# Performance work log

Measured on AMD Instinct MI355X. Metric: run time of the kernel, lower is better.

The kernel has to match this reference:

```python
import jax, jax.numpy as jnp
import numpy as np
import math

HEADS = 12
D_MODEL = 768
D_K = D_MODEL // HEADS


def setup_inputs() -> dict:
    key = jax.random.key(0)
    ks = jax.random.split(key, 11)
    B, S, D = 2, 2048, D_MODEL
    p = 0.02
    return {
        "query": jax.random.normal(ks[0], (B, S, D), jnp.float32),
        "key": jax.random.normal(ks[1], (B, S, D), jnp.float32),
        "value": jax.random.normal(ks[2], (B, S, D), jnp.float32),
        "Wq": jax.random.normal(ks[3], (D, D), jnp.float32) * p,
        "bq": jax.random.normal(ks[4], (D,), jnp.float32) * p,
        "Wk": jax.random.normal(ks[5], (D, D), jnp.float32) * p,
        "bk": jax.random.normal(ks[6], (D,), jnp.float32) * p,
        "Wv": jax.random.normal(ks[7], (D, D), jnp.float32) * p,
        "bv": jax.random.normal(ks[8], (D,), jnp.float32) * p,
        "Wo": jax.random.normal(ks[9], (D, D), jnp.float32) * p,
        "bo": jax.random.normal(ks[10], (D,), jnp.float32) * p,
    }


def reference(query, key, value, Wq, bq, Wk, bk, Wv, bv, Wo, bo):
    B, S, D = query.shape
    scale = 1.0 / math.sqrt(D_K)
    # Linear projections then split into heads: [B,S,H,Dk]
    q = (query @ Wq + bq).reshape(B, S, HEADS, D_K)
    k = (key @ Wk + bk).reshape(B, S, HEADS, D_K)
    v = (value @ Wv + bv).reshape(B, S, HEADS, D_K)
    # Full score tensor [B, i, j, H]
    scores = jnp.einsum('bihd,bjhd->bijh', q, k) * scale
    # Faithful to source: nn.Softmax(dim=1) over [b,i,j,h] -> query axis i
    attn = jax.nn.softmax(scores, axis=1)
    # dropout_prob=0 (inference/deterministic reference)
    x = jnp.einsum('bijh,bjhd->bihd', attn, v).reshape(B, S, D)
    return x @ Wo + bo
```

## Files before the change

### kernel.cpp

```cpp
#include <hip/hip_runtime.h>
#include <stdint.h>

#define HEADS 12
#define DK 64
#define DM 768
#define BT 2
#define SEQ 2048
#define ROWS (BT*SEQ)

typedef __bf16 bf16x4 __attribute__((ext_vector_type(4)));
typedef __bf16 bf16x8 __attribute__((ext_vector_type(8)));
typedef float f32x4 __attribute__((ext_vector_type(4)));

#define SCL2 0.18033688011112042f

__device__ __forceinline__ float exp2fast(float x) {
#if __has_builtin(__builtin_amdgcn_exp2f)
    return __builtin_amdgcn_exp2f(x);
#else
    return exp2f(x);
#endif
}
__device__ __forceinline__ float log2fast(float x) {
#if __has_builtin(__builtin_amdgcn_logf)
    return __builtin_amdgcn_logf(x);
#else
    return log2f(x);
#endif
}

__device__ __forceinline__ uint16_t f2bf(float f) {
    union { float f; uint32_t u; } v; v.f = f;
    uint32_t u = v.u;
    return (uint16_t)((u + 0x7FFFu + ((u >> 16) & 1u)) >> 16);
}

union U8 { uint16_t u[8]; bf16x8 v; float4 f; };

__device__ __forceinline__ bf16x8 cat44(bf16x4 lo, bf16x4 hi) {
    bf16x8 f;
    f[0] = lo[0]; f[1] = lo[1]; f[2] = lo[2]; f[3] = lo[3];
    f[4] = hi[0]; f[5] = hi[1]; f[6] = hi[2]; f[7] = hi[3];
    return f;
}

__device__ __forceinline__ bf16x8 ldfrag(const char* p) {
    bf16x4 lo = *(const bf16x4*)p;
    bf16x4 hi = *(const bf16x4*)(p + 32);
    return cat44(lo, hi);
}

__device__ __forceinline__ bf16x8 ldswz(const char* base, int row, int ks, int q) {
    int ulo = (ks * 4 + (q >> 1)) ^ (row & 7);
    int uhi = (ks * 4 + 2 + (q >> 1)) ^ (row & 7);
    return cat44(*(const bf16x4*)(base + row * 128 + ulo * 16 + (q & 1) * 8),
                 *(const bf16x4*)(base + row * 128 + uhi * 16 + (q & 1) * 8));
}

typedef __attribute__((address_space(3))) void lds_vp;
typedef const __attribute__((address_space(1))) void gbl_vp;
__device__ __forceinline__ void gload16(const void* g, void* l) {
    __builtin_amdgcn_global_load_lds((gbl_vp*)g, (lds_vp*)l, 16, 0, 0);
}

__global__ __launch_bounds__(256) void k_transpose(const float* __restrict__ Wq,
                                                   const float* __restrict__ Wk,
                                                   const float* __restrict__ Wv,
                                                   const float* __restrict__ Wo,
                                                   uint16_t* __restrict__ Wqt,
                                                   uint16_t* __restrict__ Wkt,
                                                   uint16_t* __restrict__ Wvt,
                                                   uint16_t* __restrict__ Wot) {
    __shared__ float t[32][33];
    int z = blockIdx.z;
    const float* W = (z == 0) ? Wq : (z == 1) ? Wk : (z == 2) ? Wv : Wo;
    uint16_t* Wt = (z == 0) ? Wqt : (z == 1) ? Wkt : (z == 2) ? Wvt : Wot;
    int bx = blockIdx.x * 32;
    int by = blockIdx.y * 32;
    int tx = threadIdx.x & 31, ty = threadIdx.x >> 5;
#pragma unroll
    for (int r = 0; r < 32; r += 8)
        t[ty + r][tx] = W[(size_t)(bx + ty + r) * DM + by + tx];
    __syncthreads();
#pragma unroll
    for (int r = 0; r < 32; r += 8)
        Wt[(size_t)(by + ty + r) * DM + bx + tx] = f2bf(t[tx][ty + r]);
}

__global__ __launch_bounds__(256) void k_gemm_qkv(const float* __restrict__ Aq,
                                                  const float* __restrict__ Ak,
                                                  const float* __restrict__ Av,
                                                  const uint16_t* __restrict__ Wt,
                                                  const float* __restrict__ bq,
                                                  const float* __restrict__ bk,
                                                  const float* __restrict__ bv,
                                                  uint16_t* __restrict__ Qm,
                                                  uint16_t* __restrict__ Km,
                                                  uint16_t* __restrict__ VT) {
    __shared__ char smem[2 * 2 * 128 * 80];
    const int z = blockIdx.z;
    const float* A = (z == 0) ? Aq : (z == 1) ? Ak : Av;
    const uint16_t* Bt = Wt + (size_t)z * DM * DM;
    const float* bias = (z == 0) ? bq : (z == 1) ? bk : bv;
    const int tid = threadIdx.x, lane = tid & 63, w = tid >> 6;
    const int q = lane >> 4, r16 = lane & 15;
    const int mtile = blockIdx.y * 128, ntile = blockIdx.x * 128;
    const int wm = (w >> 1) * 64, wn = (w & 1) * 64;
    const int srow = tid >> 1, shalf = tid & 1;
    const float* ap = A + (size_t)(mtile + srow) * DM + shalf * 16;
    const uint16_t* bp = Bt + (size_t)(ntile + srow) * DM + shalf * 16;
    f32x4 acc[4][4] = {};
    float4 ra0 = *(const float4*)(ap + 0);
    float4 ra1 = *(const float4*)(ap + 4);
    float4 ra2 = *(const float4*)(ap + 8);
    float4 ra3 = *(const float4*)(ap + 12);
    float4 rb0 = *(const float4*)bp;
    float4 rb1 = *(const float4*)((const char*)bp + 16);
    for (int t = 0; t < 24; ++t) {
        char* As = smem + (t & 1) * 20480;
        char* Bs = As + 10240;
        U8 pk0, pk1;
        pk0.u[0] = f2bf(ra0.x); pk0.u[1] = f2bf(ra0.y); pk0.u[2] = f2bf(ra0.z); pk0.u[3] = f2bf(ra0.w);
        pk0.u[4] = f2bf(ra1.x); pk0.u[5] = f2bf(ra1.y); pk0.u[6] = f2bf(ra1.z); pk0.u[7] = f2bf(ra1.w);
        pk1.u[0] = f2bf(ra2.x); pk1.u[1] = f2bf(ra2.y); pk1.u[2] = f2bf(ra2.z); pk1.u[3] = f2bf(ra2.w);
        pk1.u[4] = f2bf(ra3.x); pk1.u[5] = f2bf(ra3.y); pk1.u[6] = f2bf(ra3.z); pk1.u[7] = f2bf(ra3.w);
        *(float4*)(As + srow * 80 + shalf * 32) = pk0.f;
        *(float4*)(As + srow * 80 + shalf * 32 + 16) = pk1.f;
        *(float4*)(Bs + srow * 80 + shalf * 32) = rb0;
        *(float4*)(Bs + srow * 80 + shalf * 32 + 16) = rb1;
        if (t < 23) {
            const float* ap2 = ap + (t + 1) * 32;
            ra0 = *(const float4*)(ap2 + 0);
            ra1 = *(const float4*)(ap2 + 4);
            ra2 = *(const float4*)(ap2 + 8);
            ra3 = *(const float4*)(ap2 + 12);
            const uint16_t* bp2 = bp + (t + 1) * 32;
            rb0 = *(const float4*)bp2;
            rb1 = *(const float4*)((const char*)bp2 + 16);
        }
        __syncthreads();
        bf16x8 af[4], bfr[4];
#pragma unroll
        for (int i = 0; i < 4; i++) {
            af[i] = ldfrag(As + (wm + i * 16 + r16) * 80 + q * 8);
            bfr[i] = ldfrag(Bs + (wn + i * 16 + r16) * 80 + q * 8);
        }
#pragma unroll
        for (int mi = 0; mi < 4; mi++)
#pragma unroll
            for (int ni = 0; ni < 4; ni++)
                acc[mi][ni] = __builtin_amdgcn_mfma_f32_16x16x32_bf16(
                    af[mi], bfr[ni], acc[mi][ni], 0, 0, 0);
    }
    if (z < 2) {
        uint16_t* out = (z == 0) ? Qm : Km;
#pragma unroll
        for (int ni = 0; ni < 4; ni++) {
            int n = ntile + wn + ni * 16 + r16;
            float bv2 = bias[n];
#pragma unroll
            for (int mi = 0; mi < 4; mi++)
#pragma unroll
                for (int r = 0; r < 4; r++) {
                    int m = mtile + wm + mi * 16 + 4 * q + r;
                    out[(size_t)m * DM + n] = f2bf(acc[mi][ni][r] + bv2);
                }
        }
    } else {
#pragma unroll
        for (int ni = 0; ni < 4; ni++) {
            int n = ntile + wn + ni * 16 + r16;
            int h = n >> 6, dk = n & 63;
            float bv2 = bias[n];
#pragma unroll
            for (int mi = 0; mi < 4; mi++) {
                int mbase = mtile + wm + mi * 16 + 4 * q;
                int b = mbase >> 11, s = mbase & 2047;
                ushort4 o;
                o.x = f2bf(acc[mi][ni][0] + bv2);
                o.y = f2bf(acc[mi][ni][1] + bv2);
                o.z = f2bf(acc[mi][ni][2] + bv2);
                o.w = f2bf(acc[mi][ni][3] + bv2);
                *(ushort4*)(VT + ((size_t)((b * HEADS + h) * DK + dk)) * SEQ + s) = o;
            }
        }
    }
}

__global__ __launch_bounds__(256) void k_gemm_o(const uint16_t* __restrict__ A,
                                                const uint16_t* __restrict__ Bt,
                                                const float* __restrict__ bias,
                                                float* __restrict__ C) {
    __shared__ char smem[2 * 2 * 128 * 80];
    const int tid = threadIdx.x, lane = tid & 63, w = tid >> 6;
    const int q = lane >> 4, r16 = lane & 15;
    const int mtile = blockIdx.y * 128, ntile = blockIdx.x * 128;
    const int wm = (w >> 1) * 64, wn = (w & 1) * 64;
    const int srow = tid >> 1, shalf = tid & 1;
    const uint16_t* ap = A + (size_t)(mtile + srow) * DM + shalf * 16;
    const uint16_t* bp = Bt + (size_t)(ntile + srow) * DM + shalf * 16;
    f32x4 acc[4][4] = {};
    float4 ra0 = *(const float4*)ap;
    float4 ra1 = *(const float4*)((const char*)ap + 16);
    float4 rb0 = *(const float4*)bp;
    float4 rb1 = *(const float4*)((const char*)bp + 16);
    for (int t = 0; t < 24; ++t) {
        char* As = smem + (t & 1) * 20480;
        char* Bs = As + 10240;
        *(float4*)(As + srow * 80 + shalf * 32) = ra0;
        *(float4*)(As + srow * 80 + shalf * 32 + 16) = ra1;
        *(float4*)(Bs + srow * 80 + shalf * 32) = rb0;
        *(float4*)(Bs + srow * 80 + shalf * 32 + 16) = rb1;
        if (t < 23) {
            const uint16_t* ap2 = ap + (t + 1) * 32;
            ra0 = *(const float4*)ap2;
            ra1 = *(const float4*)((const char*)ap2 + 16);
            const uint16_t* bp2 = bp + (t + 1) * 32;
            rb0 = *(const float4*)bp2;
            rb1 = *(const float4*)((const char*)bp2 + 16);
        }
        __syncthreads();
        bf16x8 af[4], bfr[4];
#pragma unroll
        for (int i = 0; i < 4; i++) {
            af[i] = ldfrag(As + (wm + i * 16 + r16) * 80 + q * 8);
            bfr[i] = ldfrag(Bs + (wn + i * 16 + r16) * 80 + q * 8);
        }
#pragma unroll
        for (int mi = 0; mi < 4; mi++)
#pragma unroll
            for (int ni = 0; ni < 4; ni++)
                acc[mi][ni] = __builtin_amdgcn_mfma_f32_16x16x32_bf16(
                    af[mi], bfr[ni], acc[mi][ni], 0, 0, 0);
    }
#pragma unroll
    for (int ni = 0; ni < 4; ni++) {
        int n = ntile + wn + ni * 16 + r16;
        float bv = bias[n];
#pragma unroll
        for (int mi = 0; mi < 4; mi++)
#pragma unroll
            for (int r = 0; r < 4; r++) {
                int m = mtile + wm + mi * 16 + 4 * q + r;
                C[(size_t)m * DM + n] = acc[mi][ni][r] + bv;
            }
    }
}

__global__ __launch_bounds__(256, 4) void k_stats(const uint16_t* __restrict__ Qm,
                                                  const uint16_t* __restrict__ Km,
                                                  float* __restrict__ L2buf) {
    __shared__ char lds[4 * 8192];
    const int tid = threadIdx.x, lane = tid & 63, w = tid >> 6;
    const int q = lane >> 4, r16 = lane & 15;
    const int bh = blockIdx.y, b = bh / HEADS, h = bh % HEADS;
    const int j0 = blockIdx.x * 128 + w * 32;
    const uint16_t* Qbase = Qm + (size_t)b * SEQ * DM + h * DK;
    const uint16_t* Kbase = Km + (size_t)(b * SEQ + blockIdx.x * 128) * DM + h * DK;

#pragma unroll
    for (int c = 0; c < 4; c++) {
        int n = c * 256 + tid, row = n >> 3, u = n & 7;
        gload16(Kbase + (size_t)row * DM + ((u ^ (row & 7)) * 8), lds + n * 16);
    }
    asm volatile("s_waitcnt vmcnt(0)" ::: "memory");
    __syncthreads();
    bf16x8 kf[2][2];
#pragma unroll
    for (int jf = 0; jf < 2; jf++)
#pragma unroll
        for (int ks = 0; ks < 2; ks++)
            kf[jf][ks] = ldswz(lds, w * 32 + jf * 16 + r16, ks, q);
    __syncthreads();

    auto stage = [&](int tt) {
        char* buf = lds + (tt & 3) * 8192;
        int i1 = (tt & 31) * 64;
#pragma unroll
        for (int c = 0; c < 2; c++) {
            int n = c * 256 + tid, row = n >> 3, u = n & 7;
            gload16(Qbase + (size_t)(i1 + row) * DM + ((u ^ (row & 7)) * 8), buf + n * 16);
        }
    };
    stage(0); stage(1);
    float Zs[2][4] = {};
    for (int t = 0; t < 32; ++t) {
        stage((t + 2) & 31);
        asm volatile("s_waitcnt vmcnt(4)" ::: "memory");
        __builtin_amdgcn_sched_barrier(0);
        __builtin_amdgcn_s_barrier();
        const char* Qs = lds + (t & 3) * 8192;
#pragma unroll
        for (int f = 0; f < 4; f++) {
            bf16x8 qfr[2];
#pragma unroll
            for (int ks = 0; ks < 2; ks++) qfr[ks] = ldswz(Qs, f * 16 + r16, ks, q);
            f32x4 st[2] = {};
#pragma unroll
            for (int jf = 0; jf < 2; jf++)
#pragma unroll
                for (int ks = 0; ks < 2; ks++)
                    st[jf] = __builtin_amdgcn_mfma_f32_16x16x32_bf16(kf[jf][ks], qfr[ks], st[jf], 0, 0, 0);
#pragma unroll
            for (int jf = 0; jf < 2; jf++)
#pragma unroll
                for (int r = 0; r < 4; r++)
                    Zs[jf][r] += exp2fast(st[jf][r] * SCL2);
        }
    }
    asm volatile("s_waitcnt vmcnt(0)" ::: "memory");
#pragma unroll
    for (int jf = 0; jf < 2; jf++)
#pragma unroll
        for (int r = 0; r < 4; r++) {
            float e = Zs[jf][r];
#pragma unroll
            for (int m = 1; m < 16; m <<= 1) e += __shfl_xor(e, m);
            if (r16 == 0)
                L2buf[(size_t)bh * SEQ + j0 + jf * 16 + 4 * q + r] = -log2fast(e);
        }
}

__global__ __launch_bounds__(256, 2) void k_attn(const uint16_t* __restrict__ Qm,
                                                 const uint16_t* __restrict__ Km,
                                                 const uint16_t* __restrict__ VT,
                                                 const float* __restrict__ L2,
                                                 uint16_t* __restrict__ Xm) {
    __shared__ char lds[4 * 16384 + 8192];
    char* L2s = lds + 65536;
    const int tid = threadIdx.x, lane = tid & 63, w = tid >> 6;
    const int q = lane >> 4, r16 = lane & 15;
    const int bh = blockIdx.y, b = bh / HEADS, h = bh % HEADS;
    const int iblk = blockIdx.x * 128;
    const uint16_t* Qbase = Qm + (size_t)(b * SEQ + iblk) * DM + h * DK;
    const uint16_t* Kbase = Km + (size_t)b * SEQ * DM + h * DK;
    const uint16_t* VTb = VT + (size_t)bh * DK * SEQ;
    const float* L2b = L2 + (size_t)bh * SEQ;

    {
        int o = tid * 32;
        *(float4*)(L2s + o) = *(const float4*)((const char*)L2b + o);
        *(float4*)(L2s + o + 16) = *(const float4*)((const char*)L2b + o + 16);
    }
#pragma unroll
    for (int c = 0; c < 4; c++) {
        int n = c * 256 + tid, row = n >> 3, u = n & 7;
        gload16(Qbase + (size_t)row * DM + ((u ^ (row & 7)) * 8), lds + n * 16);
    }
    asm volatile("s_waitcnt vmcnt(0)" ::: "memory");
    __syncthreads();
    bf16x8 qf[2][2];
#pragma unroll
    for (int ig = 0; ig < 2; ig++)
#pragma unroll
        for (int ks = 0; ks < 2; ks++)
            qf[ig][ks] = ldswz(lds, w * 32 + ig * 16 + r16, ks, q);
    __syncthreads();

    auto stage = [&](int tt) {
        char* buf = lds + (tt & 3) * 16384;
        int js1 = (tt & 31) * 64;
#pragma unroll
        for (int c = 0; c < 2; c++) {
            int n = c * 256 + tid, row = n >> 3, u = n & 7;
            gload16(Kbase + (size_t)(js1 + row) * DM + ((u ^ (row & 7)) * 8), buf + n * 16);
            gload16(VTb + (size_t)row * SEQ + js1 + ((u ^ (row & 7)) * 8), buf + 8192 + n * 16);
        }
    };
    stage(0); stage(1);
    f32x4 xacc[4][2] = {};
    for (int t = 0; t < 32; ++t) {
        stage((t + 2) & 31);
        asm volatile("s_waitcnt vmcnt(8)" ::: "memory");
        __builtin_amdgcn_sched_barrier(0);
        __builtin_amdgcn_s_barrier();
        const char* Ks = lds + (t & 3) * 16384;
        const char* Vs = Ks + 8192;
        const int js = t * 64;
        bf16x8 kf[4][2], vf[4][2];
#pragma unroll
        for (int jf = 0; jf < 4; jf++)
#pragma unroll
            for (int ks = 0; ks < 2; ks++)
                kf[jf][ks] = ldswz(Ks, jf * 16 + r16, ks, q);
#pragma unroll
        for (int dc = 0; dc < 4; dc++)
#pragma unroll
            for (int c = 0; c < 2; c++)
                vf[dc][c] = ldswz(Vs, dc * 16 + r16, c, q);
        float l2a[4][4];
#pragma unroll
        for (int jf = 0; jf < 4; jf++) {
            float4 lv = *(const float4*)(L2s + (js + jf * 16 + 4 * q) * 4);
            l2a[jf][0] = lv.x; l2a[jf][1] = lv.y; l2a[jf][2] = lv.z; l2a[jf][3] = lv.w;
        }
#pragma unroll
        for (int ig = 0; ig < 2; ig++) {
            f32x4 st[4] = {};
#pragma unroll
            for (int jf = 0; jf < 4; jf++)
#pragma unroll
                for (int ks = 0; ks < 2; ks++)
                    st[jf] = __builtin_amdgcn_mfma_f32_16x16x32_bf16(kf[jf][ks], qf[ig][ks], st[jf], 0, 0, 0);
            bf16x8 pb[2];
#pragma unroll
            for (int c = 0; c < 2; c++) {
                U8 t8;
#pragma unroll
                for (int r = 0; r < 4; r++) {
                    t8.u[r]     = f2bf(exp2fast(st[2 * c][r] * SCL2 + l2a[2 * c][r]));
                    t8.u[4 + r] = f2bf(exp2fast(st[2 * c + 1][r] * SCL2 + l2a[2 * c + 1][r]));
                }
                pb[c] = t8.v;
            }
#pragma unroll
            for (int dc = 0; dc < 4; dc++)
#pragma unroll
                for (int c = 0; c < 2; c++)
                    xacc[dc][ig] = __builtin_amdgcn_mfma_f32_16x16x32_bf16(vf[dc][c], pb[c], xacc[dc][ig], 0, 0, 0);
        }
    }
    asm volatile("s_waitcnt vmcnt(0)" ::: "memory");
    __syncthreads();
    char* xr = lds + w * 4608;
#pragma unroll
    for (int dc = 0; dc < 4; dc++)
#pragma unroll
        for (int ig = 0; ig < 2; ig++) {
            bf16x4 pk;
            pk[0] = (__bf16)xacc[dc][ig][0];
            pk[1] = (__bf16)xacc[dc][ig][1];
            pk[2] = (__bf16)xacc[dc][ig][2];
            pk[3] = (__bf16)xacc[dc][ig][3];
            *(bf16x4*)(xr + (ig * 16 + r16) * 144 + (dc * 16 + 4 * q) * 2) = pk;
        }
    __syncthreads();
#pragma unroll
    for (int cc = 0; cc < 4; cc++) {
        int uidx = cc * 64 + lane;
        int row = uidx >> 3, seg = uidx & 7;
        *(float4*)(Xm + (size_t)(b * SEQ + iblk + w * 32 + row) * DM + h * DK + seg * 8) =
            *(const float4*)(xr + row * 144 + seg * 16);
    }
}

extern "C" void kernel_launch(void* const* d_in, const int* in_sizes, int n_in,
                              void* d_out, int out_size, void* d_ws, size_t ws_size,
                              hipStream_t stream) {
    const float* query = (const float*)d_in[0];
    const float* key = (const float*)d_in[1];
    const float* value = (const float*)d_in[2];
    const float* Wq = (const float*)d_in[3];
    const float* bq = (const float*)d_in[4];
    const float* Wk = (const float*)d_in[5];
    const float* bk = (const float*)d_in[6];
    const float* Wv = (const float*)d_in[7];
    const float* bv = (const float*)d_in[8];
    const float* Wo = (const float*)d_in[9];
    const float* bo = (const float*)d_in[10];
    float* out = (float*)d_out;
    char* ws = (char*)d_ws;

    const size_t SZ = (size_t)ROWS * DM * 2;
    const size_t WSZ = (size_t)DM * DM * 2;
    uint16_t* Qm = (uint16_t*)(ws + 0 * SZ);
    uint16_t* Km = (uint16_t*)(ws + 1 * SZ);
    uint16_t* VT = (uint16_t*)(ws + 2 * SZ);
    uint16_t* Xm = (uint16_t*)(ws + 3 * SZ);
    uint16_t* Wqt = (uint16_t*)(ws + 4 * SZ);
    uint16_t* Wkt = (uint16_t*)(ws + 4 * SZ + WSZ);
    uint16_t* Wvt = (uint16_t*)(ws + 4 * SZ + 2 * WSZ);
    uint16_t* Wot = (uint16_t*)(ws + 4 * SZ + 3 * WSZ);
    float* L2buf = (float*)(ws + 4 * SZ + 4 * WSZ);

    k_transpose<<<dim3(24, 24, 4), 256, 0, stream>>>(Wq, Wk, Wv, Wo, Wqt, Wkt, Wvt, Wot);
    k_gemm_qkv<<<dim3(6, 32, 3), 256, 0, stream>>>(query, key, value, Wqt, bq, bk, bv, Qm, Km, VT);
    k_stats<<<dim3(16, 24), 256, 0, stream>>>(Qm, Km, L2buf);
    k_attn<<<dim3(16, 24), 256, 0, stream>>>(Qm, Km, VT, L2buf, Xm);
    k_gemm_o<<<dim3(6, 32), 256, 0, stream>>>(Xm, Wot, bo, out);
}
```

Baseline: 256.2 us.

## Split attention and stats over key halves, fold normalization into V

The column-softmax stats kernel and the attention kernel are each split in two along the sequence, launching grids of 768 blocks instead of 384 for more parallelism. Normalization moves out of the exp: a new kernel scales V^T by the reciprocal of the summed partial Z, so the attention loop skips the per-element L2 add and its LDS staging. Attention writes two fp32 partial outputs, which the output GEMM sums and converts to bf16 while loading. Buffering goes from four stages to three with s_setprio hints. The cost is an extra kernel launch, more fp32 traffic for the partials, and bf16 rounding of the rescaled V.

```diff
diff --git a/kernel.cpp b/kernel.cpp
--- a/kernel.cpp
+++ b/kernel.cpp
@@ -21,11 +21,11 @@
     return exp2f(x);
 #endif
 }
-__device__ __forceinline__ float log2fast(float x) {
-#if __has_builtin(__builtin_amdgcn_logf)
-    return __builtin_amdgcn_logf(x);
+__device__ __forceinline__ float rcpfast(float x) {
+#if __has_builtin(__builtin_amdgcn_rcpf)
+    return __builtin_amdgcn_rcpf(x);
 #else
-    return log2f(x);
+    return 1.0f / x;
 #endif
 }
 
@@ -33,6 +33,10 @@
     union { float f; uint32_t u; } v; v.f = f;
     uint32_t u = v.u;
     return (uint16_t)((u + 0x7FFFu + ((u >> 16) & 1u)) >> 16);
+}
+__device__ __forceinline__ float bf2f(uint16_t u) {
+    union { uint32_t u; float f; } v; v.u = ((uint32_t)u) << 16;
+    return v.f;
 }
 
 union U8 { uint16_t u[8]; bf16x8 v; float4 f; };
@@ -187,7 +191,8 @@
     }
 }
 
-__global__ __launch_bounds__(256) void k_gemm_o(const uint16_t* __restrict__ A,
+__global__ __launch_bounds__(256) void k_gemm_o(const float* __restrict__ Xp0,
+                                                const float* __restrict__ Xp1,
                                                 const uint16_t* __restrict__ Bt,
                                                 const float* __restrict__ bias,
                                                 float* __restrict__ C) {
@@ -197,24 +202,39 @@
     const int mtile = blockIdx.y * 128, ntile = blockIdx.x * 128;
     const int wm = (w >> 1) * 64, wn = (w & 1) * 64;
     const int srow = tid >> 1, shalf = tid & 1;
-    const uint16_t* ap = A + (size_t)(mtile + srow) * DM + shalf * 16;
+    const float* x0 = Xp0 + (size_t)(mtile + srow) * DM + shalf * 16;
+    const float* x1 = Xp1 + (size_t)(mtile + srow) * DM + shalf * 16;
     const uint16_t* bp = Bt + (size_t)(ntile + srow) * DM + shalf * 16;
     f32x4 acc[4][4] = {};
-    float4 ra0 = *(const float4*)ap;
-    float4 ra1 = *(const float4*)((const char*)ap + 16);
+    float4 ra0 = *(const float4*)(x0 + 0), ra1 = *(const float4*)(x0 + 4);
+    float4 ra2 = *(const float4*)(x0 + 8), ra3 = *(const float4*)(x0 + 12);
+    float4 rc0 = *(const float4*)(x1 + 0), rc1 = *(const float4*)(x1 + 4);
+    float4 rc2 = *(const float4*)(x1 + 8), rc3 = *(const float4*)(x1 + 12);
     float4 rb0 = *(const float4*)bp;
     float4 rb1 = *(const float4*)((const char*)bp + 16);
     for (int t = 0; t < 24; ++t) {
         char* As = smem + (t & 1) * 20480;
         char* Bs = As + 10240;
-        *(float4*)(As + srow * 80 + shalf * 32) = ra0;
-        *(float4*)(As + srow * 80 + shalf * 32 + 16) = ra1;
+        U8 pk0, pk1;
+        pk0.u[0] = f2bf(ra0.x + rc0.x); pk0.u[1] = f2bf(ra0.y + rc0.y);
+        pk0.u[2] = f2bf(ra0.z + rc0.z); pk0.u[3] = f2bf(ra0.w + rc0.w);
+        pk0.u[4] = f2bf(ra1.x + rc1.x); pk0.u[5] = f2bf(ra1.y + rc1.y);
+        pk0.u[6] = f2bf(ra1.z + rc1.z); pk0.u[7] = f2bf(ra1.w + rc1.w);
+        pk1.u[0] = f2bf(ra2.x + rc2.x); pk1.u[1] = f2bf(ra2.y + rc2.y);
+        pk1.u[2] = f2bf(ra2.z + rc2.z); pk1.u[3] = f2bf(ra2.w + rc2.w);
+        pk1.u[4] = f2bf(ra3.x + rc3.x); pk1.u[5] = f2bf(ra3.y + rc3.y);
+        pk1.u[6] = f2bf(ra3.z + rc3.z); pk1.u[7] = f2bf(ra3.w + rc3.w);
+        *(float4*)(As + srow * 80 + shalf * 32) = pk0.f;
+        *(float4*)(As + srow * 80 + shalf * 32 + 16) = pk1.f;
         *(float4*)(Bs + srow * 80 + shalf * 32) = rb0;
         *(float4*)(Bs + srow * 80 + shalf * 32 + 16) = rb1;
         if (t < 23) {
-            const uint16_t* ap2 = ap + (t + 1) * 32;
-            ra0 = *(const float4*)ap2;
-            ra1 = *(const float4*)((const char*)ap2 + 16);
+            const float* x0n = x0 + (t + 1) * 32;
+            const float* x1n = x1 + (t + 1) * 32;
+            ra0 = *(const float4*)(x0n + 0); ra1 = *(const float4*)(x0n + 4);
+            ra2 = *(const float4*)(x0n + 8); ra3 = *(const float4*)(x0n + 12);
+            rc0 = *(const float4*)(x1n + 0); rc1 = *(const float4*)(x1n + 4);
+            rc2 = *(const float4*)(x1n + 8); rc3 = *(const float4*)(x1n + 12);
             const uint16_t* bp2 = bp + (t + 1) * 32;
             rb0 = *(const float4*)bp2;
             rb1 = *(const float4*)((const char*)bp2 + 16);
@@ -247,15 +267,16 @@
     }
 }
 
-__global__ __launch_bounds__(256, 4) void k_stats(const uint16_t* __restrict__ Qm,
+__global__ __launch_bounds__(256, 3) void k_stats(const uint16_t* __restrict__ Qm,
                                                   const uint16_t* __restrict__ Km,
-                                                  float* __restrict__ L2buf) {
-    __shared__ char lds[4 * 8192];
+                                                  float* __restrict__ Zpart) {
+    __shared__ char lds[3 * 8192];
     const int tid = threadIdx.x, lane = tid & 63, w = tid >> 6;
     const int q = lane >> 4, r16 = lane & 15;
     const int bh = blockIdx.y, b = bh / HEADS, h = bh % HEADS;
     const int j0 = blockIdx.x * 128 + w * 32;
-    const uint16_t* Qbase = Qm + (size_t)b * SEQ * DM + h * DK;
+    const int ihalf = blockIdx.z;
+    const uint16_t* Qbase = Qm + (size_t)(b * SEQ + ihalf * 1024) * DM + h * DK;
     const uint16_t* Kbase = Km + (size_t)(b * SEQ + blockIdx.x * 128) * DM + h * DK;
 
 #pragma unroll
@@ -273,28 +294,30 @@
             kf[jf][ks] = ldswz(lds, w * 32 + jf * 16 + r16, ks, q);
     __syncthreads();
 
-    auto stage = [&](int tt) {
-        char* buf = lds + (tt & 3) * 8192;
-        int i1 = (tt & 31) * 64;
+    auto stageQ = [&](char* buf, int tt) {
+        int i1 = (tt & 15) * 64;
 #pragma unroll
         for (int c = 0; c < 2; c++) {
             int n = c * 256 + tid, row = n >> 3, u = n & 7;
             gload16(Qbase + (size_t)(i1 + row) * DM + ((u ^ (row & 7)) * 8), buf + n * 16);
         }
     };
-    stage(0); stage(1);
+    char* p0 = lds;
+    char* p1 = lds + 8192;
+    char* p2 = lds + 16384;
+    stageQ(p0, 0);
     float Zs[2][4] = {};
-    for (int t = 0; t < 32; ++t) {
-        stage((t + 2) & 31);
-        asm volatile("s_waitcnt vmcnt(4)" ::: "memory");
+    for (int t = 0; t < 16; ++t) {
+        stageQ(p1, t + 1);
+        asm volatile("s_waitcnt vmcnt(2)" ::: "memory");
         __builtin_amdgcn_sched_barrier(0);
         __builtin_amdgcn_s_barrier();
-        const char* Qs = lds + (t & 3) * 8192;
+        __builtin_amdgcn_s_setprio(1);
 #pragma unroll
         for (int f = 0; f < 4; f++) {
             bf16x8 qfr[2];
 #pragma unroll
-            for (int ks = 0; ks < 2; ks++) qfr[ks] = ldswz(Qs, f * 16 + r16, ks, q);
+            for (int ks = 0; ks < 2; ks++) qfr[ks] = ldswz(p0, f * 16 + r16, ks, q);
             f32x4 st[2] = {};
 #pragma unroll
             for (int jf = 0; jf < 2; jf++)
@@ -307,6 +330,8 @@
                 for (int r = 0; r < 4; r++)
                     Zs[jf][r] += exp2fast(st[jf][r] * SCL2);
         }
+        __builtin_amdgcn_s_setprio(0);
+        char* tp = p0; p0 = p1; p1 = p2; p2 = tp;
     }
     asm volatile("s_waitcnt vmcnt(0)" ::: "memory");
 #pragma unroll
@@ -317,31 +342,51 @@
 #pragma unroll
             for (int m = 1; m < 16; m <<= 1) e += __shfl_xor(e, m);
             if (r16 == 0)
-                L2buf[(size_t)bh * SEQ + j0 + jf * 16 + 4 * q + r] = -log2fast(e);
-        }
-}
-
-__global__ __launch_bounds__(256, 2) void k_attn(const uint16_t* __restrict__ Qm,
+                Zpart[((size_t)ihalf * 24 + bh) * SEQ + j0 + jf * 16 + 4 * q + r] = e;
+        }
+}
+
+__global__ __launch_bounds__(256) void k_vscale(uint16_t* __restrict__ VT,
+                                                const float* __restrict__ Zpart) {
+    size_t t = (size_t)blockIdx.x * 256 + threadIdx.x;
+    size_t base = t * 8;
+    int rowid = (int)(base >> 11);
+    int bh = rowid >> 6;
+    int s0 = (int)(base & 2047);
+    const float* z0p = Zpart + (size_t)bh * SEQ + s0;
+    const float* z1p = Zpart + (size_t)24 * SEQ + (size_t)bh * SEQ + s0;
+    float4 a0 = *(const float4*)z0p, a1 = *(const float4*)(z0p + 4);
+    float4 b0 = *(const float4*)z1p, b1 = *(const float4*)(z1p + 4);
+    ushort4 va = *(ushort4*)(VT + base);
+    ushort4 vb = *(ushort4*)(VT + base + 4);
+    ushort4 oa, oc;
+    oa.x = f2bf(bf2f(va.x) * rcpfast(a0.x + b0.x));
+    oa.y = f2bf(bf2f(va.y) * rcpfast(a0.y + b0.y));
+    oa.z = f2bf(bf2f(va.z) * rcpfast(a0.z + b0.z));
+    oa.w = f2bf(bf2f(va.w) * rcpfast(a0.w + b0.w));
+    oc.x = f2bf(bf2f(vb.x) * rcpfast(a1.x + b1.x));
+    oc.y = f2bf(bf2f(vb.y) * rcpfast(a1.y + b1.y));
+    oc.z = f2bf(bf2f(vb.z) * rcpfast(a1.z + b1.z));
+    oc.w = f2bf(bf2f(vb.w) * rcpfast(a1.w + b1.w));
+    *(ushort4*)(VT + base) = oa;
+    *(ushort4*)(VT + base + 4) = oc;
+}
+
+__global__ __launch_bounds__(256, 3) void k_attn(const uint16_t* __restrict__ Qm,
                                                  const uint16_t* __restrict__ Km,
                                                  const uint16_t* __restrict__ VT,
-                                                 const float* __restrict__ L2,
-                                                 uint16_t* __restrict__ Xm) {
-    __shared__ char lds[4 * 16384 + 8192];
-    char* L2s = lds + 65536;
+                                                 float* __restrict__ Xp) {
+    __shared__ char lds[3 * 16384];
     const int tid = threadIdx.x, lane = tid & 63, w = tid >> 6;
     const int q = lane >> 4, r16 = lane & 15;
     const int bh = blockIdx.y, b = bh / HEADS, h = bh % HEADS;
     const int iblk = blockIdx.x * 128;
+    const int jbase = blockIdx.z * 1024;
     const uint16_t* Qbase = Qm + (size_t)(b * SEQ + iblk) * DM + h * DK;
-    const uint16_t* Kbase = Km + (size_t)b * SEQ * DM + h * DK;
-    const uint16_t* VTb = VT + (size_t)bh * DK * SEQ;
-    const float* L2b = L2 + (size_t)bh * SEQ;
-
-    {
-        int o = tid * 32;
-        *(float4*)(L2s + o) = *(const float4*)((const char*)L2b + o);
-        *(float4*)(L2s + o + 16) = *(const float4*)((const char*)L2b + o + 16);
-    }
+    const uint16_t* Kbase = Km + (size_t)(b * SEQ + jbase) * DM + h * DK;
+    const uint16_t* VTb = VT + (size_t)bh * DK * SEQ + jbase;
+    float* Xout = Xp + (size_t)blockIdx.z * ROWS * DM;
+
 #pragma unroll
     for (int c = 0; c < 4; c++) {
         int n = c * 256 + tid, row = n >> 3, u = n & 7;
@@ -357,9 +402,8 @@
             qf[ig][ks] = ldswz(lds, w * 32 + ig * 16 + r16, ks, q);
     __syncthreads();
 
-    auto stage = [&](int tt) {
-        char* buf = lds + (tt & 3) * 16384;
-        int js1 = (tt & 31) * 64;
+    auto stageKV = [&](char* buf, int tt) {
+        int js1 = (tt & 15) * 64;
 #pragma unroll
         for (int c = 0; c < 2; c++) {
             int n = c * 256 + tid, row = n >> 3, u = n & 7;
@@ -367,16 +411,19 @@
             gload16(VTb + (size_t)row * SEQ + js1 + ((u ^ (row & 7)) * 8), buf + 8192 + n * 16);
         }
     };
-    stage(0); stage(1);
+    char* p0 = lds;
+    char* p1 = lds + 16384;
+    char* p2 = lds + 32768;
+    stageKV(p0, 0);
     f32x4 xacc[4][2] = {};
-    for (int t = 0; t < 32; ++t) {
-        stage((t + 2) & 31);
-        asm volatile("s_waitcnt vmcnt(8)" ::: "memory");
+    for (int t = 0; t < 16; ++t) {
+        stageKV(p1, t + 1);
+        asm volatile("s_waitcnt vmcnt(4)" ::: "memory");
         __builtin_amdgcn_sched_barrier(0);
         __builtin_amdgcn_s_barrier();
-        const char* Ks = lds + (t & 3) * 16384;
-        const char* Vs = Ks + 8192;
-        const int js = t * 64;
+        __builtin_amdgcn_s_setprio(1);
+        const char* Ks = p0;
+        const char* Vs = p0 + 8192;
         bf16x8 kf[4][2], vf[4][2];
 #pragma unroll
         for (int jf = 0; jf < 4; jf++)
@@ -388,12 +435,6 @@
 #pragma unroll
             for (int c = 0; c < 2; c++)
                 vf[dc][c] = ldswz(Vs, dc * 16 + r16, c, q);
-        float l2a[4][4];
-#pragma unroll
-        for (int jf = 0; jf < 4; jf++) {
-            float4 lv = *(const float4*)(L2s + (js + jf * 16 + 4 * q) * 4);
-            l2a[jf][0] = lv.x; l2a[jf][1] = lv.y; l2a[jf][2] = lv.z; l2a[jf][3] = lv.w;
-        }
 #pragma unroll
         for (int ig = 0; ig < 2; ig++) {
             f32x4 st[4] = {};
@@ -408,8 +449,8 @@
                 U8 t8;
 #pragma unroll
                 for (int r = 0; r < 4; r++) {
-                    t8.u[r]     = f2bf(exp2fast(st[2 * c][r] * SCL2 + l2a[2 * c][r]));
-                    t8.u[4 + r] = f2bf(exp2fast(st[2 * c + 1][r] * SCL2 + l2a[2 * c + 1][r]));
+                    t8.u[r]     = f2bf(exp2fast(st[2 * c][r] * SCL2));
+                    t8.u[4 + r] = f2bf(exp2fast(st[2 * c + 1][r] * SCL2));
                 }
                 pb[c] = t8.v;
             }
@@ -419,28 +460,24 @@
                 for (int c = 0; c < 2; c++)
                     xacc[dc][ig] = __builtin_amdgcn_mfma_f32_16x16x32_bf16(vf[dc][c], pb[c], xacc[dc][ig], 0, 0, 0);
         }
+        __builtin_amdgcn_s_setprio(0);
+        char* tp = p0; p0 = p1; p1 = p2; p2 = tp;
     }
     asm volatile("s_waitcnt vmcnt(0)" ::: "memory");
     __syncthreads();
-    char* xr = lds + w * 4608;
+    char* xr = lds + w * 8448;
 #pragma unroll
     for (int dc = 0; dc < 4; dc++)
 #pragma unroll
-        for (int ig = 0; ig < 2; ig++) {
-            bf16x4 pk;
-            pk[0] = (__bf16)xacc[dc][ig][0];
-            pk[1] = (__bf16)xacc[dc][ig][1];
-            pk[2] = (__bf16)xacc[dc][ig][2];
-            pk[3] = (__bf16)xacc[dc][ig][3];
-            *(bf16x4*)(xr + (ig * 16 + r16) * 144 + (dc * 16 + 4 * q) * 2) = pk;
-        }
-    __syncthreads();
-#pragma unroll
-    for (int cc = 0; cc < 4; cc++) {
+        for (int ig = 0; ig < 2; ig++)
+            *(f32x4*)(xr + (ig * 16 + r16) * 264 + (dc * 16 + 4 * q) * 4) = xacc[dc][ig];
+    __syncthreads();
+#pragma unroll
+    for (int cc = 0; cc < 8; cc++) {
         int uidx = cc * 64 + lane;
-        int row = uidx >> 3, seg = uidx & 7;
-        *(float4*)(Xm + (size_t)(b * SEQ + iblk + w * 32 + row) * DM + h * DK + seg * 8) =
-            *(const float4*)(xr + row * 144 + seg * 16);
+        int row = uidx >> 4, seg = uidx & 15;
+        *(float4*)(Xout + (size_t)(b * SEQ + iblk + w * 32 + row) * DM + h * DK + seg * 4) =
+            *(const float4*)(xr + row * 264 + seg * 16);
     }
 }
 
@@ -463,19 +500,23 @@
 
     const size_t SZ = (size_t)ROWS * DM * 2;
     const size_t WSZ = (size_t)DM * DM * 2;
+    const size_t XSZ = (size_t)ROWS * DM * 4;
     uint16_t* Qm = (uint16_t*)(ws + 0 * SZ);
     uint16_t* Km = (uint16_t*)(ws + 1 * SZ);
     uint16_t* VT = (uint16_t*)(ws + 2 * SZ);
-    uint16_t* Xm = (uint16_t*)(ws + 3 * SZ);
-    uint16_t* Wqt = (uint16_t*)(ws + 4 * SZ);
-    uint16_t* Wkt = (uint16_t*)(ws + 4 * SZ + WSZ);
-    uint16_t* Wvt = (uint16_t*)(ws + 4 * SZ + 2 * WSZ);
-    uint16_t* Wot = (uint16_t*)(ws + 4 * SZ + 3 * WSZ);
-    float* L2buf = (float*)(ws + 4 * SZ + 4 * WSZ);
+    uint16_t* Wqt = (uint16_t*)(ws + 3 * SZ);
+    uint16_t* Wkt = (uint16_t*)(ws + 3 * SZ + WSZ);
+    uint16_t* Wvt = (uint16_t*)(ws + 3 * SZ + 2 * WSZ);
+    uint16_t* Wot = (uint16_t*)(ws + 3 * SZ + 3 * WSZ);
+    float* Zpart = (float*)(ws + 3 * SZ + 4 * WSZ);
+    char* xbase = ws + 3 * SZ + 4 * WSZ + 2 * 24 * SEQ * 4;
+    float* Xp0 = (float*)xbase;
+    float* Xp1 = (float*)(xbase + XSZ);
 
     k_transpose<<<dim3(24, 24, 4), 256, 0, stream>>>(Wq, Wk, Wv, Wo, Wqt, Wkt, Wvt, Wot);
     k_gemm_qkv<<<dim3(6, 32, 3), 256, 0, stream>>>(query, key, value, Wqt, bq, bk, bv, Qm, Km, VT);
-    k_stats<<<dim3(16, 24), 256, 0, stream>>>(Qm, Km, L2buf);
-    k_attn<<<dim3(16, 24), 256, 0, stream>>>(Qm, Km, VT, L2buf, Xm);
-    k_gemm_o<<<dim3(6, 32), 256, 0, stream>>>(Xm, Wot, bo, out);
-}
+    k_stats<<<dim3(16, 24, 2), 256, 0, stream>>>(Qm, Km, Zpart);
+    k_vscale<<<dim3(1536), 256, 0, stream>>>(VT, Zpart);
+    k_attn<<<dim3(16, 24, 2), 256, 0, stream>>>(Qm, Km, VT, Xp0);
+    k_gemm_o<<<dim3(6, 32), 256, 0, stream>>>(Xp0, Xp1, Wot, bo, out);
+}
```

Result: faster. 242.6 us (-5.3%).
